# Performance work log

Measured on AMD Instinct MI355X. Metric: run time of the kernel, lower is better.

Reference implementation:

```python
import jax, jax.numpy as jnp
from jax import lax
import numpy as np
import math

B, C, Hs, Ws = 2, 512, 48, 48
HW = Hs * Ws            # 2304; also m (compress_ratio = 1)
M = HW
GROUPS = 256
GS = M // GROUPS        # 9, exact split
ALPHA = 0.05
MAXITER = 43
TOL = B * HW * 1e-7     # torch: z0.numel()*tol with z0 of shape [N, HW]
EPS = 1e-5
POWER_ITERS = 100


def _make_A():
    # random projection: num_ones = round(sqrt(m)) ones per column, rows L2-normalized
    rng = np.random.RandomState(0)
    num_ones = int(round(math.sqrt(M)))  # 48
    A = np.zeros((M, HW), dtype=np.float32)
    rows = np.argsort(rng.rand(HW, M), axis=1)[:, :num_ones]  # [HW, num_ones]
    A[rows.ravel(), np.repeat(np.arange(HW), num_ones)] = 1.0
    A /= np.maximum(np.sqrt((A ** 2).sum(axis=1, keepdims=True)), 1e-12)
    return jnp.asarray(A)


def setup_inputs() -> dict:
    key = jax.random.key(0)
    ks = jax.random.split(key, 10)
    f32 = jnp.float32
    d = {
        'content': jax.random.normal(ks[0], (B, C, Hs, Ws), f32),
        'style': jax.random.normal(ks[1], (B, C, Hs, Ws), f32),
        'content_key': jax.random.normal(ks[2], (B, C, Hs, Ws), f32),
        'style_key': jax.random.normal(ks[3], (B, C, Hs, Ws), f32),
        'f_w': jax.random.normal(ks[4], (C, C), f32) * 0.02,
        'f_b': jnp.zeros((C,), f32),
        'g_w': jax.random.normal(ks[5], (C, C), f32) * 0.02,
        'g_b': jnp.zeros((C,), f32),
        'h_w': jax.random.normal(ks[6], (C, C), f32) * 0.02,
        'h_b': jnp.zeros((C,), f32),
        'A': _make_A(),
    }
    return d


def _conv1x1(x, w, b):
    # nn.Conv2d(Cin, Cout, 1): [b,c,h,w] x [o,c] + bias
    return jnp.einsum('bchw,oc->bohw', x, w) + b[None, :, None, None]


def _softshrink(x, lam):
    return jnp.sign(x) * jnp.maximum(jnp.abs(x) - lam, 0.0)


def _forward(content, style, content_key, style_key, f_w, f_b, g_w, g_b, h_w, h_b, A):
    Fq = _conv1x1(content_key, f_w, f_b).reshape(B, C, HW).transpose(0, 2, 1)  # [b,HWc,Ck]
    G = _conv1x1(style_key, g_w, g_b).reshape(B, C, HW)                        # [b,Ck,HWs]
    Hh = _conv1x1(style, h_w, h_b).reshape(B, C, HW)
    # HW <= max_sample: no subsampling branch
    style_flat = Hh.transpose(0, 2, 1)                                         # [b,HWs,C]
    S = jax.nn.softmax(jnp.einsum('bqc,bck->bqk', Fq, G), axis=-1)             # [b,HWc,HWs]
    mean = jnp.einsum('bqk,bkc->bqc', S, style_flat)                           # weighted mean
    std = jnp.sqrt(jax.nn.relu(jnp.einsum('bqk,bkc->bqc', S, style_flat ** 2) - mean ** 2))
    mean = mean.transpose(0, 2, 1)  # [b,C,HW]
    std = std.transpose(0, 2, 1)
    # random projection along spatial dim: feat @ A^T
    proj = lambda f: jnp.einsum('mh,bch->bcm', A, f)
    mean_c = proj(mean)
    std_c = proj(std)
    cont_c = proj(content.reshape(B, C, HW))
    # per-group mean/variance norm (256 equal groups of GS along compressed dim)
    g = cont_c.reshape(B, C, GROUPS, GS)
    mu = g.mean(axis=-1, keepdims=True)
    var = g.var(axis=-1, ddof=1, keepdims=True)  # torch var is unbiased
    normed = (g - mu) / jnp.sqrt(var + EPS)
    x = (normed * std_c.reshape(B, C, GROUPS, GS)
         + mean_c.reshape(B, C, GROUPS, GS)).reshape(B, C, M)
    # FISTA sparse coding: min 0.5||z A^T - x||^2 + alpha |z|_1
    Ad = lax.stop_gradient(A)
    WtW = Ad.T @ Ad
    v = jnp.full((HW,), 1.0 / math.sqrt(HW), jnp.float32)
    def _pi(v, _):
        w = WtW @ v
        return w / jnp.linalg.norm(w), None
    v, _ = lax.scan(_pi, v, None, length=POWER_ITERS)
    L = v @ (WtW @ v)  # largest eigenvalue of A^T A
    lr = 1.0 / L
    z0 = jnp.zeros((B, C, HW), x.dtype)

    def step(carry, _):
        z, y, t, done = carry
        resid = jnp.einsum('bch,mh->bcm', y, A) - x   # y @ A^T - x
        grad = jnp.einsum('bcm,mh->bch', resid, A)    # resid @ A
        zn = _softshrink(y - lr * grad, ALPHA * lr)
        diff = jnp.abs(z - zn).sum()
        tn = (1.0 + jnp.sqrt(1.0 + 4.0 * t * t)) / 2.0
        yn = zn + (t - 1.0) / tn * (zn - z)
        z2 = jnp.where(done, z, zn)
        y2 = jnp.where(done, y, yn)
        t2 = jnp.where(done, t, tn)
        done2 = done | (diff <= TOL)
        return (z2, y2, t2, done2), None

    (z, _, _, _), _ = lax.scan(step, (z0, z0, jnp.float32(1.0), jnp.array(False)),
                               None, length=MAXITER)
    return z.reshape(B, C, Hs, Ws)


def reference(content, style, content_key, style_key, f_w, f_b, g_w, g_b, h_w, h_b, A):
    return _forward(content, style, content_key, style_key,
                    f_w, f_b, g_w, g_b, h_w, h_b, A)
```

## Files before the change

kernel.cpp:

```cpp
#include <hip/hip_runtime.h>
#include <math.h>

#define TPB 256

typedef _Float16 f16;
typedef _Float16 half8 __attribute__((ext_vector_type(8)));
typedef _Float16 f16x2 __attribute__((ext_vector_type(2)));
typedef _Float16 f16x4 __attribute__((ext_vector_type(4)));
typedef float floatx4 __attribute__((ext_vector_type(4)));

static constexpr int CDIM = 512;
static constexpr int HWD = 2304;
static constexpr float ALPHA = 0.05f;
static constexpr float TOLF = 4.608e-4f;

enum { EPI_F32 = 0, EPI_F16BIASN = 1, EPI_F16BIASM = 2, EPI_F16 = 3,
       EPI_WTW = 4, EPI_MEANSTD = 5, EPI_FISTA = 6 };

__device__ __forceinline__ bool fista_done(const float* __restrict__ diffArr, int iter) {
    bool done = false;
    for (int j = 0; j < iter; ++j) done = done || (diffArr[j] <= TOLF);
    return done;
}

__device__ __forceinline__ void gload_lds(const f16* g, f16* l) {
#if __has_builtin(__builtin_amdgcn_global_load_lds)
    __builtin_amdgcn_global_load_lds(
        (__attribute__((address_space(1))) void*)(g),
        (__attribute__((address_space(3))) void*)(l), 16, 0, 0);
#else
    *(int4*)l = *(const int4*)g;
#endif
}

template<int EPI, int MF>
__global__ __launch_bounds__(TPB, 3) void sgemm(
    const f16* __restrict__ A, long a_bs, int lda,
    const f16* __restrict__ B, long b_bs, int ldb,
    void* __restrict__ C0, long c_bs, int ldc,
    void* __restrict__ C1,
    int K,
    const float* __restrict__ bias,
    const float* __restrict__ xAf,
    float* __restrict__ zc, float* __restrict__ zp, f16* __restrict__ yhp,
    const float* __restrict__ lrs, float coefPrev, float coefCur,
    float* __restrict__ diffArr, int iter)
{
    if (EPI == EPI_FISTA) {
        if (iter > 0 && fista_done(diffArr, iter)) return;
    }
    constexpr int ASZ = MF * 32 * 64;
    constexpr int BSZ = 64 * 64;
    __shared__ alignas(16) f16 As[2 * ASZ];
    __shared__ alignas(16) f16 Bs[2 * BSZ];
    const int tid = threadIdx.x;
    const int wid = tid >> 6, lane = tid & 63;
    const int wr = wid >> 1, wc = wid & 1;

    const int gx = gridDim.x, gy = gridDim.y;
    const int nwg = gx * gy;
    const int d = blockIdx.y * gx + blockIdx.x;
    const int q = nwg >> 3, r = nwg & 7;
    const int xcd = d & 7, rest = d >> 3;
    const int wgid = (xcd < r ? xcd * (q + 1) : r * (q + 1) + (xcd - r) * q) + rest;
    const int bx = wgid / gy, by = wgid % gy;

    const int m0 = by * (MF * 32), n0 = bx << 6;
    const f16* Ab = A + (long)blockIdx.z * a_bs;
    const f16* Bb = B + (long)blockIdx.z * b_bs;

    floatx4 acc[MF][2] = {};
    floatx4 acc2[MF][2] = {};

    const int rl = lane & 15, kg = lane >> 4;
    const int lrow = lane >> 3;
    const int gs = (lane & 7) ^ lrow;

    const int nt = K >> 6;

    auto STAGE = [&](int t, int buf) {
        const long k0 = (long)t << 6;
        f16* Ad = As + buf * ASZ;
        f16* Bd = Bs + buf * BSZ;
        #pragma unroll
        for (int p = 0; p < MF; ++p) {
            const int c = wid * MF + p;
            const int R = c * 8 + lrow;
            gload_lds(Ab + (long)(m0 + R) * lda + k0 + gs * 8, Ad + c * 512);
        }
        #pragma unroll
        for (int p = 0; p < 2; ++p) {
            const int c = wid * 2 + p;
            const int R = c * 8 + lrow;
            gload_lds(Bb + (long)(n0 + R) * ldb + k0 + gs * 8, Bd + c * 512);
        }
    };

    STAGE(0, 0);
    __syncthreads();
    for (int t = 0; t < nt; ++t) {
        const int cur = t & 1;
        if (t + 1 < nt) STAGE(t + 1, cur ^ 1);
        const f16* Ac = As + cur * ASZ;
        const f16* Bc = Bs + cur * BSZ;
        #pragma unroll
        for (int kk = 0; kk < 2; ++kk) {
            const int j = kk * 4 + kg;
            half8 af[MF], bf[2];
            #pragma unroll
            for (int f = 0; f < MF; ++f) {
                const int rowa = wr * (MF * 16) + f * 16 + rl;
                af[f] = *(const half8*)&Ac[rowa * 64 + ((j ^ (rowa & 7)) * 8)];
            }
            #pragma unroll
            for (int f = 0; f < 2; ++f) {
                const int rowb = wc * 32 + f * 16 + rl;
                bf[f] = *(const half8*)&Bc[rowb * 64 + ((j ^ (rowb & 7)) * 8)];
            }
            #pragma unroll
            for (int fi = 0; fi < MF; ++fi) {
                #pragma unroll
                for (int fj = 0; fj < 2; ++fj) {
                    acc[fi][fj] = __builtin_amdgcn_mfma_f32_16x16x32_f16(af[fi], bf[fj], acc[fi][fj], 0, 0, 0);
                    if constexpr (EPI == EPI_MEANSTD) {
                        half8 bq = bf[fj] * bf[fj];
                        acc2[fi][fj] = __builtin_amdgcn_mfma_f32_16x16x32_f16(af[fi], bq, acc2[fi][fj], 0, 0, 0);
                    }
                }
            }
        }
        __syncthreads();
    }

    const int rg = lane >> 4;
    const int bz = blockIdx.z;
    float loc = 0.f;
    float lr = 0.f, sh = 0.f;
    if constexpr (EPI == EPI_FISTA) { lr = lrs[0]; sh = lrs[1]; }

    #pragma unroll
    for (int fi = 0; fi < MF; ++fi) {
        #pragma unroll
        for (int fj = 0; fj < 2; ++fj) {
            #pragma unroll
            for (int r2 = 0; r2 < 4; ++r2) {
                const int row = m0 + wr * (MF * 16) + fi * 16 + rg * 4 + r2;
                const int col = n0 + wc * 32 + fj * 16 + rl;
                const float v = acc[fi][fj][r2];
                if constexpr (EPI == EPI_F32) {
                    ((float*)C0)[bz * c_bs + (long)row * ldc + col] = v;
                } else if constexpr (EPI == EPI_F16BIASN) {
                    ((f16*)C0)[bz * c_bs + (long)row * ldc + col] = (f16)(v + bias[col]);
                } else if constexpr (EPI == EPI_F16BIASM) {
                    ((f16*)C0)[bz * c_bs + (long)row * ldc + col] = (f16)(v + bias[row]);
                } else if constexpr (EPI == EPI_F16) {
                    ((f16*)C0)[bz * c_bs + (long)row * ldc + col] = (f16)v;
                } else if constexpr (EPI == EPI_WTW) {
                    ((float*)C0)[(long)row * ldc + col] = v;
                    ((f16*)C1)[(long)row * ldc + col] = (f16)v;
                } else if constexpr (EPI == EPI_MEANSTD) {
                    const float m_ = v;
                    float s2 = acc2[fi][fj][r2] - m_ * m_;
                    const long o = ((long)bz * CDIM + col) * HWD + row;
                    ((f16*)C0)[o] = (f16)m_;
                    ((f16*)C1)[o] = (f16)sqrtf(s2 > 0.f ? s2 : 0.f);
                } else {
                    const long off = (long)row * HWD + col;
                    const float zk = zc[off];
                    const float zkm = zp[off];
                    const float ykf = zk + coefPrev * (zk - zkm);
                    const float grad = v - xAf[off];
                    const float p = ykf - lr * grad;
                    const float ap = fabsf(p) - sh;
                    const float zn = ap > 0.f ? copysignf(ap, p) : 0.f;
                    zp[off] = zn;
                    yhp[off] = (f16)(zn + coefCur * (zn - zk));
                    loc += fabsf(zn - zk);
                }
            }
        }
    }
    if constexpr (EPI == EPI_FISTA) {
        __shared__ float red[TPB];
        red[tid] = loc; __syncthreads();
        for (int s = 128; s > 0; s >>= 1) { if (tid < s) red[tid] += red[tid + s]; __syncthreads(); }
        if (tid == 0) atomicAdd(&diffArr[iter], red[0]);
    }
}

__global__ __launch_bounds__(TPB) void tcvt(const float* __restrict__ in, long in_bs,
                                            f16* __restrict__ out, long out_bs, int R, int Cc) {
    __shared__ float t[32][33];
    const int b = blockIdx.z;
    const int r0 = blockIdx.y << 5, c0 = blockIdx.x << 5;
    const int tx = threadIdx.x & 31, ty = threadIdx.x >> 5;
    const float* ib = in + (long)b * in_bs;
    #pragma unroll
    for (int p = 0; p < 4; ++p) {
        const int r = ty + p * 8;
        t[r][tx] = ib[(long)(r0 + r) * Cc + c0 + tx];
    }
    __syncthreads();
    f16* ob = out + (long)b * out_bs;
    #pragma unroll
    for (int p = 0; p < 4; ++p) {
        const int c = ty + p * 8;
        ob[(long)(c0 + c) * R + r0 + tx] = (f16)t[tx][c];
    }
}

__global__ void cvt16(const float4* __restrict__ in, f16x4* __restrict__ out, long n4) {
    long i = (long)blockIdx.x * blockDim.x + threadIdx.x;
    const long st = (long)gridDim.x * blockDim.x;
    for (; i < n4; i += st) {
        const float4 v = in[i];
        f16x4 o; o.x = (f16)v.x; o.y = (f16)v.y; o.z = (f16)v.z; o.w = (f16)v.w;
        out[i] = o;
    }
}

__global__ __launch_bounds__(TPB) void softmax_h(const float* __restrict__ Sf, f16* __restrict__ Sh) {
    __shared__ float row[HWD];
    __shared__ float red[TPB];
    const long base = (long)blockIdx.x * HWD;
    const int tid = threadIdx.x;
    float mx = -3.4e38f;
    for (int i = tid; i < HWD; i += TPB) { const float v = Sf[base + i]; row[i] = v; mx = fmaxf(mx, v); }
    red[tid] = mx; __syncthreads();
    for (int s = 128; s > 0; s >>= 1) { if (tid < s) red[tid] = fmaxf(red[tid], red[tid + s]); __syncthreads(); }
    mx = red[0]; __syncthreads();
    float sum = 0.f;
    for (int i = tid; i < HWD; i += TPB) { const float e = expf(row[i] - mx); row[i] = e; sum += e; }
    red[tid] = sum; __syncthreads();
    for (int s = 128; s > 0; s >>= 1) { if (tid < s) red[tid] += red[tid + s]; __syncthreads(); }
    const float inv = 1.0f / red[0];
    for (int i = tid; i < HWD; i += TPB) Sh[base + i] = (f16)(row[i] * inv);
}

__global__ __launch_bounds__(TPB) void groupnorm_x(const float* __restrict__ contc,
                                                   const float* __restrict__ meanc,
                                                   const float* __restrict__ stdc,
                                                   f16* __restrict__ xh) {
    const long base = (long)blockIdx.x * HWD + (long)threadIdx.x * 9;
    float v[9];
    float mu = 0.f;
    #pragma unroll
    for (int j = 0; j < 9; ++j) { v[j] = contc[base + j]; mu += v[j]; }
    mu *= (1.0f / 9.0f);
    float var = 0.f;
    #pragma unroll
    for (int j = 0; j < 9; ++j) { const float d = v[j] - mu; var += d * d; }
    var *= (1.0f / 8.0f);
    const float rs = 1.0f / sqrtf(var + 1e-5f);
    #pragma unroll
    for (int j = 0; j < 9; ++j)
        xh[base + j] = (f16)((v[j] - mu) * rs * (float)stdc[base + j] + (float)meanc[base + j]);
}

__global__ __launch_bounds__(TPB) void matvec_h(const f16* __restrict__ Wm,
                                                const float* __restrict__ win,
                                                float* __restrict__ wout) {
    __shared__ float red[TPB];
    const int tid = threadIdx.x;
    float s = 0.f;
    for (int i = tid; i < HWD; i += TPB) { const float v = win[i]; s += v * v; }
    red[tid] = s; __syncthreads();
    for (int st = 128; st > 0; st >>= 1) { if (tid < st) red[tid] += red[tid + st]; __syncthreads(); }
    const float ninv = rsqrtf(red[0]);
    const int row = (blockIdx.x << 2) + (tid >> 6);
    const int lane = tid & 63;
    const f16x2* wr2 = (const f16x2*)(Wm + (long)row * HWD);
    float d = 0.f;
    for (int j = lane; j < HWD / 2; j += 64) {
        const f16x2 p = wr2[j];
        d += (float)p.x * win[2 * j] + (float)p.y * win[2 * j + 1];
    }
    #pragma unroll
    for (int o = 32; o > 0; o >>= 1) d += __shfl_down(d, o);
    if (lane == 0) wout[row] = d * ninv;
}

__global__ __launch_bounds__(TPB) void kernelL(const float* __restrict__ Wf,
                                               const float* __restrict__ w,
                                               float* __restrict__ Lnum, float* __restrict__ Lden) {
    __shared__ float red[TPB];
    const int tid = threadIdx.x;
    const int row = (blockIdx.x << 2) + (tid >> 6);
    const int lane = tid & 63;
    const float* wr = Wf + (long)row * HWD;
    float d = 0.f;
    for (int j = lane; j < HWD; j += 64) d += wr[j] * w[j];
    #pragma unroll
    for (int o = 32; o > 0; o >>= 1) d += __shfl_down(d, o);
    red[tid] = (lane == 0) ? d * w[row] : 0.f;
    __syncthreads();
    for (int s = 128; s > 0; s >>= 1) { if (tid < s) red[tid] += red[tid + s]; __syncthreads(); }
    if (tid == 0) atomicAdd(Lnum, red[0]);
    if (blockIdx.x == 0) {
        __syncthreads();
        float s2 = 0.f;
        for (int i = tid; i < HWD; i += TPB) { const float v = w[i]; s2 += v * v; }
        red[tid] = s2; __syncthreads();
        for (int s = 128; s > 0; s >>= 1) { if (tid < s) red[tid] += red[tid + s]; __syncthreads(); }
        if (tid == 0) *Lden = red[0];
    }
}

__global__ void lr_fin(const float* __restrict__ Lnum, const float* __restrict__ Lden,
                       float* __restrict__ lrs) {
    const float lr = Lden[0] / Lnum[0];
    lrs[0] = lr;
    lrs[1] = ALPHA * lr;
}

__global__ void init_small(float* __restrict__ wvec, float* __restrict__ diffArr,
                           float* __restrict__ Lnum) {
    const int tid = threadIdx.x;
    for (int i = tid; i < HWD; i += TPB) wvec[i] = (float)(1.0 / 48.0);
    if (tid < 43) diffArr[tid] = 0.f;
    if (tid == 64) Lnum[0] = 0.f;
}

__global__ void zero_kernel(float4* __restrict__ p, long n4) {
    long i = (long)blockIdx.x * blockDim.x + threadIdx.x;
    const long st = (long)gridDim.x * blockDim.x;
    for (; i < n4; i += st) p[i] = make_float4(0.f, 0.f, 0.f, 0.f);
}

__global__ void copy_fista(const float4* __restrict__ zfA, const float4* __restrict__ zfB,
                           float4* __restrict__ out, const float* __restrict__ diffArr, long n4) {
    int last = 42;
    for (int j = 0; j < 43; ++j) { if (diffArr[j] <= TOLF) { last = j; break; } }
    const float4* src = (last & 1) ? zfA : zfB;
    long i = (long)blockIdx.x * blockDim.x + threadIdx.x;
    const long st = (long)gridDim.x * blockDim.x;
    for (; i < n4; i += st) out[i] = src[i];
}

extern "C" void kernel_launch(void* const* d_in, const int* in_sizes, int n_in,
                              void* d_out, int out_size, void* d_ws, size_t ws_size,
                              hipStream_t stream) {
    (void)in_sizes; (void)n_in; (void)out_size;
    const float* content = (const float*)d_in[0];
    const float* style   = (const float*)d_in[1];
    const float* ckey    = (const float*)d_in[2];
    const float* skey    = (const float*)d_in[3];
    const float* f_w = (const float*)d_in[4];
    const float* f_b = (const float*)d_in[5];
    const float* g_w = (const float*)d_in[6];
    const float* g_b = (const float*)d_in[7];
    const float* h_w = (const float*)d_in[8];
    const float* h_b = (const float*)d_in[9];
    const float* Amat = (const float*)d_in[10];

    if (ws_size < 79500000) return;
    char* W = (char*)d_ws;

    const long E16 = (long)HWD * CDIM;
    const long EHH = (long)HWD * HWD;
    f16*  ckeyT = (f16*)(W + 0);
    f16*  skeyT = (f16*)(W + 4718592);
    f16*  styleT= (f16*)(W + 9437184);
    float* Sf   = (float*)(W + 0);
    f16*  Ah    = (f16*)(W + 0);
    f16*  At    = (f16*)(W + 10616832);
    f16*  Wh    = (f16*)(W + 21233664);
    f16*  W4h   = (f16*)(W + 31850496);
    f16*  W2h   = (f16*)(W + 0);
    float* contc= (float*)(W + 21233664);
    float* zfA  = (float*)(W + 0);
    float* zfB  = (float*)(W + 9437184);
    f16*  yh    = (f16*)(W + 31850496);
    f16*  Sh    = (f16*)(W + 42467328);
    float* meanc= (float*)(W + 42467328);
    float* stdc = (float*)(W + 42467328 + 9437184);
    float* Wf   = (float*)(W + 42467328);
    float* xAf  = (float*)(W + 42467328);
    f16*  Fh    = (f16*)(W + 63700992);
    f16*  Gh    = (f16*)(W + 63700992 + 4718592);
    f16*  Hh    = (f16*)(W + 63700992 + 9437184);
    f16*  meanx = (f16*)(W + 63700992);
    f16*  stdx  = (f16*)(W + 63700992 + 4718592);
    f16*  conth = (f16*)(W + 63700992 + 9437184);
    f16*  xh    = (f16*)(W + 63700992);
    float* w_a  = (float*)(W + 77856768);
    float* w_b  = (float*)(W + 77856768 + 9216);
    float* lrs  = (float*)(W + 77856768 + 18432);
    float* Lnum = (float*)(W + 77856768 + 18440);
    float* Lden = (float*)(W + 77856768 + 18444);
    float* diffArr = (float*)(W + 77856768 + 18448);
    f16*  fwh   = (f16*)(W + 77875712);
    f16*  gwh   = (f16*)(W + 77875712 + 524288);
    f16*  hwh   = (f16*)(W + 77875712 + 1048576);

    init_small<<<1, TPB, 0, stream>>>(w_a, diffArr, Lnum);

    cvt16<<<256, TPB, 0, stream>>>((const float4*)f_w, (f16x4*)fwh, (long)CDIM * CDIM / 4);
    cvt16<<<256, TPB, 0, stream>>>((const float4*)g_w, (f16x4*)gwh, (long)CDIM * CDIM / 4);
    cvt16<<<256, TPB, 0, stream>>>((const float4*)h_w, (f16x4*)hwh, (long)CDIM * CDIM / 4);
    tcvt<<<dim3(72, 16, 2), TPB, 0, stream>>>(ckey, E16, ckeyT, E16, CDIM, HWD);
    tcvt<<<dim3(72, 16, 2), TPB, 0, stream>>>(skey, E16, skeyT, E16, CDIM, HWD);
    tcvt<<<dim3(72, 16, 2), TPB, 0, stream>>>(style, E16, styleT, E16, CDIM, HWD);

    sgemm<EPI_F16BIASN, 2><<<dim3(8, 36, 2), TPB, 0, stream>>>(ckeyT, E16, CDIM, fwh, 0, CDIM,
        Fh, E16, CDIM, nullptr, CDIM, f_b, nullptr, nullptr, nullptr, nullptr, nullptr, 0.f, 0.f, nullptr, 0);
    sgemm<EPI_F16BIASN, 2><<<dim3(8, 36, 2), TPB, 0, stream>>>(skeyT, E16, CDIM, gwh, 0, CDIM,
        Gh, E16, CDIM, nullptr, CDIM, g_b, nullptr, nullptr, nullptr, nullptr, nullptr, 0.f, 0.f, nullptr, 0);
    sgemm<EPI_F16BIASM, 2><<<dim3(36, 8, 2), TPB, 0, stream>>>(hwh, 0, CDIM, styleT, E16, CDIM,
        Hh, E16, HWD, nullptr, CDIM, h_b, nullptr, nullptr, nullptr, nullptr, nullptr, 0.f, 0.f, nullptr, 0);

    sgemm<EPI_F32, 4><<<dim3(36, 18, 2), TPB, 0, stream>>>(Fh, E16, CDIM, Gh, E16, CDIM,
        Sf, EHH, HWD, nullptr, CDIM, nullptr, nullptr, nullptr, nullptr, nullptr, nullptr, 0.f, 0.f, nullptr, 0);
    softmax_h<<<2 * HWD, TPB, 0, stream>>>(Sf, Sh);

    cvt16<<<2048, TPB, 0, stream>>>((const float4*)Amat, (f16x4*)Ah, EHH / 4);
    tcvt<<<dim3(72, 72, 1), TPB, 0, stream>>>(Amat, 0, At, 0, HWD, HWD);

    sgemm<EPI_MEANSTD, 2><<<dim3(8, 36, 2), TPB, 0, stream>>>(Sh, EHH, HWD, Hh, E16, HWD,
        meanx, 0, HWD, stdx, HWD, nullptr, nullptr, nullptr, nullptr, nullptr, nullptr, 0.f, 0.f, nullptr, 0);

    cvt16<<<2048, TPB, 0, stream>>>((const float4*)content, (f16x4*)conth, (long)2 * E16 / 4);

    sgemm<EPI_F32, 2><<<dim3(36, 16, 1), TPB, 0, stream>>>(meanx, 0, HWD, Ah, 0, HWD,
        meanc, 0, HWD, nullptr, HWD, nullptr, nullptr, nullptr, nullptr, nullptr, nullptr, 0.f, 0.f, nullptr, 0);
    sgemm<EPI_F32, 2><<<dim3(36, 16, 1), TPB, 0, stream>>>(stdx, 0, HWD, Ah, 0, HWD,
        stdc, 0, HWD, nullptr, HWD, nullptr, nullptr, nullptr, nullptr, nullptr, nullptr, 0.f, 0.f, nullptr, 0);
    sgemm<EPI_F32, 2><<<dim3(36, 16, 1), TPB, 0, stream>>>(conth, 0, HWD, Ah, 0, HWD,
        contc, 0, HWD, nullptr, HWD, nullptr, nullptr, nullptr, nullptr, nullptr, nullptr, 0.f, 0.f, nullptr, 0);

    groupnorm_x<<<1024, TPB, 0, stream>>>(contc, meanc, stdc, xh);

    sgemm<EPI_WTW, 4><<<dim3(36, 18, 1), TPB, 0, stream>>>(At, 0, HWD, At, 0, HWD,
        Wf, 0, HWD, Wh, HWD, nullptr, nullptr, nullptr, nullptr, nullptr, nullptr, 0.f, 0.f, nullptr, 0);
    sgemm<EPI_F16, 4><<<dim3(36, 18, 1), TPB, 0, stream>>>(Wh, 0, HWD, Wh, 0, HWD,
        W2h, 0, HWD, nullptr, HWD, nullptr, nullptr, nullptr, nullptr, nullptr, nullptr, 0.f, 0.f, nullptr, 0);
    sgemm<EPI_F16, 4><<<dim3(36, 18, 1), TPB, 0, stream>>>(W2h, 0, HWD, W2h, 0, HWD,
        W4h, 0, HWD, nullptr, HWD, nullptr, nullptr, nullptr, nullptr, nullptr, nullptr, 0.f, 0.f, nullptr, 0);

    for (int it = 0; it < 25; ++it) {
        const float* win = (it & 1) ? w_b : w_a;
        float* wout = (it & 1) ? w_a : w_b;
        matvec_h<<<HWD / 4, TPB, 0, stream>>>(W4h, win, wout);
    }
    kernelL<<<HWD / 4, TPB, 0, stream>>>(Wf, w_b, Lnum, Lden);
    lr_fin<<<1, 1, 0, stream>>>(Lnum, Lden, lrs);

    sgemm<EPI_F32, 2><<<dim3(36, 16, 1), TPB, 0, stream>>>(xh, 0, HWD, At, 0, HWD,
        xAf, 0, HWD, nullptr, HWD, nullptr, nullptr, nullptr, nullptr, nullptr, nullptr, 0.f, 0.f, nullptr, 0);

    zero_kernel<<<1024, TPB, 0, stream>>>((float4*)zfA, E16);
    zero_kernel<<<1024, TPB, 0, stream>>>((float4*)yh, E16 / 4);

    float t = 1.0f, coefPrev = 0.0f;
    for (int it = 0; it < 43; ++it) {
        const float tn = (1.0f + sqrtf(1.0f + 4.0f * t * t)) * 0.5f;
        const float coef = (t - 1.0f) / tn;
        t = tn;
        float* zc = (it & 1) ? zfB : zfA;
        float* zp = (it & 1) ? zfA : zfB;
        sgemm<EPI_FISTA, 2><<<dim3(36, 16, 1), TPB, 0, stream>>>(yh, 0, HWD, Wh, 0, HWD,
            nullptr, 0, HWD, nullptr, HWD, nullptr, xAf, zc, zp, yh, lrs, coefPrev, coef, diffArr, it);
        coefPrev = coef;
    }

    copy_fista<<<2048, TPB, 0, stream>>>((const float4*)zfA, (const float4*)zfB,
                                         (float4*)d_out, diffArr, 2 * E16 / 4);
}
```

Before: 2.185 ms.

## Triple-buffer LDS staging with explicit vmcnt waits for deeper prefetch

The GEMM main loop changes from double-buffered global-to-LDS staging to a configurable multi-buffer pipeline, with three buffers when MF==2. It prefetches NBUF-1 tiles ahead and waits only on the oldest loads using explicit s_waitcnt vmcnt counts, replacing __syncthreads with a raw s_barrier. The aim is to hide global load latency better by keeping more loads in flight. In exchange it uses more LDS, which can reduce occupancy. The hand-written vmcnt counts must match the number of loads issued per stage, or the kernel will read data that has not arrived yet.

After: 2.167 ms. No clear change (-0.8%).

```diff
diff --git a/kernel.cpp b/kernel.cpp
--- a/kernel.cpp
+++ b/kernel.cpp
@@ -31,6 +31,19 @@
 #else
     *(int4*)l = *(const int4*)g;
 #endif
+}
+
+template<int N> __device__ __forceinline__ void vwait() {
+    if constexpr (N == 0)      asm volatile("s_waitcnt vmcnt(0)" ::: "memory");
+    else if constexpr (N == 4) asm volatile("s_waitcnt vmcnt(4)" ::: "memory");
+    else if constexpr (N == 6) asm volatile("s_waitcnt vmcnt(6)" ::: "memory");
+    else if constexpr (N == 8) asm volatile("s_waitcnt vmcnt(8)" ::: "memory");
+}
+
+__device__ __forceinline__ void barrier_f() {
+    asm volatile("" ::: "memory");
+    __builtin_amdgcn_s_barrier();
+    asm volatile("" ::: "memory");
 }
 
 template<int EPI, int MF>
@@ -51,8 +64,10 @@
     }
     constexpr int ASZ = MF * 32 * 64;
     constexpr int BSZ = 64 * 64;
-    __shared__ alignas(16) f16 As[2 * ASZ];
-    __shared__ alignas(16) f16 Bs[2 * BSZ];
+    constexpr int LCNT = MF + 2;
+    constexpr int NBUF = (MF == 2) ? 3 : 2;
+    __shared__ alignas(16) f16 As[NBUF * ASZ];
+    __shared__ alignas(16) f16 Bs[NBUF * BSZ];
     const int tid = threadIdx.x;
     const int wid = tid >> 6, lane = tid & 63;
     const int wr = wid >> 1, wc = wid & 1;
@@ -96,11 +111,18 @@
         }
     };
 
-    STAGE(0, 0);
-    __syncthreads();
+    #pragma unroll
+    for (int p = 0; p < NBUF - 1; ++p) STAGE(p, p);
+
     for (int t = 0; t < nt; ++t) {
-        const int cur = t & 1;
-        if (t + 1 < nt) STAGE(t + 1, cur ^ 1);
+        const int nxt = t + NBUF - 1;
+        if (nxt < nt) STAGE(nxt, nxt % NBUF);
+        const int rem = (nt - 1 - t < NBUF - 1) ? (nt - 1 - t) : (NBUF - 1);
+        if (rem == NBUF - 1)      vwait<(NBUF - 1) * LCNT>();
+        else if (rem == 1)        vwait<LCNT>();
+        else                      vwait<0>();
+        barrier_f();
+        const int cur = t % NBUF;
         const f16* Ac = As + cur * ASZ;
         const f16* Bc = Bs + cur * BSZ;
         #pragma unroll
@@ -129,7 +151,7 @@
                 }
             }
         }
-        __syncthreads();
+        barrier_f();
     }
 
     const int rg = lane >> 4;
```
